# Kernel optimization log

Measured on AMD Instinct MI355X. Metric: run time of the kernel, lower is better.

## Reference

```python
import jax, jax.numpy as jnp
import numpy as np

N = 100000
E = 3200000
IN_C, HID, OUT_C = 256, 32, 16


def gcn_conv(x, W, b, src, dst, n):
    """PyG GCNConv: h = D^{-1/2}(A+I)D^{-1/2} (x W) + b, self-loops already in src/dst."""
    h = x @ W  # [N, out]
    deg = jax.ops.segment_sum(jnp.ones_like(dst, dtype=h.dtype), dst, num_segments=n)
    dinv = jax.lax.rsqrt(deg)  # deg >= 1 because of self-loops
    norm = dinv[src] * dinv[dst]  # [E_all]
    msg = h[src] * norm[:, None]  # gather + normalize
    return jax.ops.segment_sum(msg, dst, num_segments=n) + b


def setup_inputs() -> dict:
    key = jax.random.key(0)
    k1, k2, k3, k4 = jax.random.split(key, 4)
    x = jax.random.normal(k1, (N, IN_C), dtype=jnp.float32)
    edge_index = jax.random.randint(k2, (2, E), 0, N, dtype=jnp.int64)
    # Glorot-ish init for weights, zero bias (as in PyG defaults)
    W1 = jax.random.normal(k3, (IN_C, HID), dtype=jnp.float32) / np.sqrt(IN_C)
    b1 = jnp.zeros((HID,), dtype=jnp.float32)
    W2 = jax.random.normal(k4, (HID, OUT_C), dtype=jnp.float32) / np.sqrt(HID)
    b2 = jnp.zeros((OUT_C,), dtype=jnp.float32)
    return {"x": x, "edge_index": edge_index, "W1": W1, "b1": b1, "W2": W2, "b2": b2}


def reference(x, edge_index, W1, b1, W2, b2):
    n = x.shape[0]
    loops = jnp.arange(n, dtype=edge_index.dtype)
    src = jnp.concatenate([edge_index[0], loops])  # add self-loops
    dst = jnp.concatenate([edge_index[1], loops])
    h = jax.nn.relu(gcn_conv(x, W1, b1, src, dst, n))
    return gcn_conv(h, W2, b2, src, dst, n)
```

## Files before the change

### kernel.cpp

```cpp
#include <hip/hip_runtime.h>

#define IN_C 256
#define HIDC 32
#define OUTC 16
#define NPB  256
#define MAXBKT 800
#define CAP  16384
#define EPB  12288
#define EPT  12

typedef __attribute__((ext_vector_type(8))) short short8;
typedef __attribute__((ext_vector_type(4))) float f32x4;
union S8U4 { short8 s; unsigned u[4]; };

__device__ __forceinline__ unsigned bf16pair(float a, float b) {
    unsigned ua = __float_as_uint(a); ua += 0x7FFF + ((ua >> 16) & 1);
    unsigned ub = __float_as_uint(b); ub += 0x7FFF + ((ub >> 16) & 1);
    return (ua >> 16) | (ub & 0xFFFF0000u);
}
__device__ __forceinline__ float bf16lo(unsigned u) { return __uint_as_float(u << 16); }
__device__ __forceinline__ float bf16hi(unsigned u) { return __uint_as_float(u & 0xFFFF0000u); }
__device__ __forceinline__ unsigned rbf(float a) {
    unsigned u = __float_as_uint(a);
    u += 0x7FFF + ((u >> 16) & 1);
    return u >> 16;
}
__device__ __forceinline__ void split8(const float* xf, short8& hi, short8& lo) {
    S8U4 H, L;
#pragma unroll
    for (int i = 0; i < 4; ++i) {
        float a = xf[2 * i], b = xf[2 * i + 1];
        unsigned ha = rbf(a), hb = rbf(b);
        float ra = a - __uint_as_float(ha << 16);
        float rb = b - __uint_as_float(hb << 16);
        H.u[i] = ha | (hb << 16);
        L.u[i] = rbf(ra) | (rbf(rb) << 16);
    }
    hi = H.s; lo = L.s;
}

__device__ __forceinline__ int edge_at(const int* __restrict__ ei, long long idx, int is64) {
    return is64 ? ei[idx << 1] : ei[idx];
}

__global__ void k_detect(const int* __restrict__ ei, int* __restrict__ flag,
                         int* __restrict__ bkt_cur, int nbkt) {
    __shared__ int nz;
    if (threadIdx.x == 0) nz = 0;
    __syncthreads();
    if (ei[2 * threadIdx.x + 1] != 0) atomicOr(&nz, 1);
    for (int i = threadIdx.x; i < nbkt; i += 256) bkt_cur[i] = i * CAP;
    __syncthreads();
    if (threadIdx.x == 0) *flag = (nz == 0) ? 1 : 0;
}

__global__ __launch_bounds__(1024) void k_bin_scatter(const int* __restrict__ ei, long long E,
                                                      const int* __restrict__ flag,
                                                      int* __restrict__ bkt_cur,
                                                      unsigned* __restrict__ packed, int nbkt) {
    __shared__ int hist[MAXBKT];
    int is64 = *flag;
    for (int i = threadIdx.x; i < nbkt; i += 1024) hist[i] = 0;
    __syncthreads();
    long long lo = (long long)blockIdx.x * EPB;
    int m = (int)((E - lo) < EPB ? (E - lo) : EPB);
    unsigned ew[EPT];
    int      eb[EPT];
#pragma unroll
    for (int j = 0; j < EPT; ++j) {
        int i = j * 1024 + (int)threadIdx.x;
        eb[j] = -1;
        if (i < m) {
            int s = edge_at(ei, lo + i, is64);
            int d = edge_at(ei, E + lo + i, is64);
            ew[j] = (unsigned)s | ((unsigned)(d & (NPB - 1)) << 20);
            eb[j] = d >> 8;
            atomicAdd(&hist[eb[j]], 1);
        }
    }
    __syncthreads();
    for (int b = threadIdx.x; b < nbkt; b += 1024) {
        int c = hist[b];
        hist[b] = c ? atomicAdd(&bkt_cur[b], c) : 0;
    }
    __syncthreads();
#pragma unroll
    for (int j = 0; j < EPT; ++j) {
        if (eb[j] >= 0) {
            int slot = atomicAdd(&hist[eb[j]], 1);
            packed[slot] = ew[j];
        }
    }
}

__global__ __launch_bounds__(256) void k_bucket_csr(const unsigned* __restrict__ packed,
                                                    const int* __restrict__ bkt_cur,
                                                    int* __restrict__ csr_src,
                                                    int* __restrict__ ptr,
                                                    int* __restrict__ cnt,
                                                    float* __restrict__ dinv, int n) {
    __shared__ int hist[NPB];
    __shared__ int off[NPB];
    hist[threadIdx.x] = 0;
    __syncthreads();
    int base = blockIdx.x * CAP;
    int m = bkt_cur[blockIdx.x] - base;
    for (int i = threadIdx.x; i < m; i += 256)
        atomicAdd(&hist[packed[base + i] >> 20], 1);
    __syncthreads();
    off[threadIdx.x] = hist[threadIdx.x];
    __syncthreads();
    for (int o = 1; o < NPB; o <<= 1) {
        int v = (threadIdx.x >= o) ? off[threadIdx.x - o] : 0;
        __syncthreads();
        off[threadIdx.x] += v;
        __syncthreads();
    }
    int node = blockIdx.x * NPB + threadIdx.x;
    {
        int exc = off[threadIdx.x] - hist[threadIdx.x];
        if (node < n) {
            ptr[node]  = base + exc;
            cnt[node]  = hist[threadIdx.x];
            dinv[node] = rsqrtf((float)hist[threadIdx.x] + 1.0f);
        }
        hist[threadIdx.x] = exc;
    }
    __syncthreads();
    for (int i = threadIdx.x; i < m; i += 256) {
        unsigned w = packed[base + i];
        int r = atomicAdd(&hist[w >> 20], 1);
        csr_src[base + r] = (int)(w & 0xFFFFF);
    }
}

__global__ void k_wfrag(const float* __restrict__ W1, unsigned short* __restrict__ wf) {
    int idx = blockIdx.x * 256 + threadIdx.x;
    if (idx >= 8 * 2 * 2 * 64) return;
    int lane = idx & 63;
    int part = (idx >> 6) & 1;
    int tile = (idx >> 7) & 1;
    int s    = idx >> 8;
    int col = tile * 16 + (lane & 15);
    int k0  = s * 32 + (lane >> 4) * 8;
#pragma unroll
    for (int j = 0; j < 8; ++j) {
        float v = W1[(long long)(k0 + j) * HIDC + col];
        unsigned h = rbf(v);
        float r = v - __uint_as_float(h << 16);
        wf[(long long)idx * 8 + j] = (unsigned short)(part == 0 ? h : rbf(r));
    }
}

__global__ __launch_bounds__(256) void k_gemm1(const float* __restrict__ x,
                                               const unsigned short* __restrict__ wf,
                                               const float* __restrict__ dinv,
                                               unsigned short* __restrict__ h1b_us, int n) {
    const int t = threadIdx.x;
    const int l = t & 63;
    const int w = t >> 6;
    const long long nb0 = (long long)blockIdx.x * 64 + w * 16;
    const int arow = l & 15;
    const int kg = l >> 4;
    const long long nodeA = nb0 + arow;
    const bool loadA = nodeA < n;
    f32x4 acc0 = {0.f, 0.f, 0.f, 0.f}, acc1 = {0.f, 0.f, 0.f, 0.f};

#pragma unroll
    for (int s = 0; s < 8; ++s) {
        float xf[8];
        if (loadA) {
            float4 v0 = *(const float4*)(x + nodeA * IN_C + s * 32 + kg * 8);
            float4 v1 = *(const float4*)(x + nodeA * IN_C + s * 32 + kg * 8 + 4);
            xf[0] = v0.x; xf[1] = v0.y; xf[2] = v0.z; xf[3] = v0.w;
            xf[4] = v1.x; xf[5] = v1.y; xf[6] = v1.z; xf[7] = v1.w;
        } else {
#pragma unroll
            for (int j = 0; j < 8; ++j) xf[j] = 0.f;
        }
        short8 ah, al;
        split8(xf, ah, al);
        const unsigned short* base = wf + ((long long)(s * 4) * 64 + l) * 8;
        short8 bh0 = *(const short8*)(base);
        short8 bl0 = *(const short8*)(base + 64 * 8);
        short8 bh1 = *(const short8*)(base + 2 * 64 * 8);
        short8 bl1 = *(const short8*)(base + 3 * 64 * 8);
        acc0 = __builtin_amdgcn_mfma_f32_16x16x32_bf16(ah, bh0, acc0, 0, 0, 0);
        acc0 = __builtin_amdgcn_mfma_f32_16x16x32_bf16(ah, bl0, acc0, 0, 0, 0);
        acc0 = __builtin_amdgcn_mfma_f32_16x16x32_bf16(al, bh0, acc0, 0, 0, 0);
        acc1 = __builtin_amdgcn_mfma_f32_16x16x32_bf16(ah, bh1, acc1, 0, 0, 0);
        acc1 = __builtin_amdgcn_mfma_f32_16x16x32_bf16(ah, bl1, acc1, 0, 0, 0);
        acc1 = __builtin_amdgcn_mfma_f32_16x16x32_bf16(al, bh1, acc1, 0, 0, 0);
    }
#pragma unroll
    for (int r = 0; r < 4; ++r) {
        long long nd = nb0 + (l >> 4) * 4 + r;
        if (nd < n) {
            float di = dinv[nd];
            h1b_us[nd * 32 + (l & 15)]      = (unsigned short)rbf(acc0[r] * di);
            h1b_us[nd * 32 + 16 + (l & 15)] = (unsigned short)rbf(acc1[r] * di);
        }
    }
}

__global__ __launch_bounds__(256) void k_agg1g2(const int* __restrict__ ptr,
                                                const int* __restrict__ cnt,
                                                const int* __restrict__ csr_src,
                                                const float* __restrict__ dinv,
                                                const unsigned* __restrict__ h1b,
                                                const float* __restrict__ b1,
                                                const float* __restrict__ W2,
                                                unsigned* __restrict__ h2b, int n) {
    __shared__ float hs[16][33];
    __shared__ float wl2[32][17];
    const int t = threadIdx.x;
    for (int i = t; i < HIDC * OUTC; i += 256) wl2[i >> 4][i & 15] = W2[i];
    const int nl = t >> 4;
    const int cp = t & 15;
    const long long node = (long long)blockIdx.x * 16 + nl;
    float vL = 0.f, vH = 0.f;
    if (node < n) {
        unsigned us = h1b[node * 16 + cp];
        float accL = bf16lo(us), accH = bf16hi(us);
        int st = ptr[node], deg = cnt[node];
        int j = 0;
        for (; j + 3 < deg; j += 4) {
            int s0 = csr_src[st + j], s1 = csr_src[st + j + 1];
            int s2 = csr_src[st + j + 2], s3 = csr_src[st + j + 3];
            unsigned u0 = h1b[(long long)s0 * 16 + cp];
            unsigned u1 = h1b[(long long)s1 * 16 + cp];
            unsigned u2 = h1b[(long long)s2 * 16 + cp];
            unsigned u3 = h1b[(long long)s3 * 16 + cp];
            accL += (bf16lo(u0) + bf16lo(u1)) + (bf16lo(u2) + bf16lo(u3));
            accH += (bf16hi(u0) + bf16hi(u1)) + (bf16hi(u2) + bf16hi(u3));
        }
        for (; j < deg; ++j) {
            unsigned u = h1b[(long long)csr_src[st + j] * 16 + cp];
            accL += bf16lo(u); accH += bf16hi(u);
        }
        float di = dinv[node];
        vL = accL * di + b1[2 * cp];
        vH = accH * di + b1[2 * cp + 1];
        vL = vL > 0.f ? vL : 0.f;
        vH = vH > 0.f ? vH : 0.f;
    }
    hs[nl][2 * cp]     = vL;
    hs[nl][2 * cp + 1] = vH;
    __syncthreads();
    if (t < 128) {
        int nl2 = t >> 3;
        int op  = t & 7;
        long long nd = (long long)blockIdx.x * 16 + nl2;
        if (nd < n) {
            float o0 = 0.f, o1 = 0.f;
#pragma unroll
            for (int k = 0; k < HIDC; ++k) {
                float h = hs[nl2][k];
                o0 = fmaf(h, wl2[k][2 * op],     o0);
                o1 = fmaf(h, wl2[k][2 * op + 1], o1);
            }
            float di = dinv[nd];
            h2b[nd * 8 + op] = bf16pair(o0 * di, o1 * di);
        }
    }
}

__global__ __launch_bounds__(256) void k_agg2csr(const int* __restrict__ ptr,
                                                 const int* __restrict__ cnt,
                                                 const int* __restrict__ csr_src,
                                                 const float* __restrict__ dinv,
                                                 const unsigned* __restrict__ h2b,
                                                 const float* __restrict__ b2,
                                                 float* __restrict__ out, int n) {
    long long g = (long long)blockIdx.x * blockDim.x + threadIdx.x;
    int node = (int)(g >> 3);
    int cp = (int)(g & 7);
    if (node >= n) return;
    unsigned us = h2b[(long long)node * 8 + cp];
    float accL = bf16lo(us), accH = bf16hi(us);
    int st = ptr[node], deg = cnt[node];
    int j = 0;
    for (; j + 3 < deg; j += 4) {
        int s0 = csr_src[st + j], s1 = csr_src[st + j + 1];
        int s2 = csr_src[st + j + 2], s3 = csr_src[st + j + 3];
        unsigned u0 = h2b[(long long)s0 * 8 + cp];
        unsigned u1 = h2b[(long long)s1 * 8 + cp];
        unsigned u2 = h2b[(long long)s2 * 8 + cp];
        unsigned u3 = h2b[(long long)s3 * 8 + cp];
        accL += (bf16lo(u0) + bf16lo(u1)) + (bf16lo(u2) + bf16lo(u3));
        accH += (bf16hi(u0) + bf16hi(u1)) + (bf16hi(u2) + bf16hi(u3));
    }
    for (; j < deg; ++j) {
        unsigned u = h2b[(long long)csr_src[st + j] * 8 + cp];
        accL += bf16lo(u); accH += bf16hi(u);
    }
    float di = dinv[node];
    *(float2*)(out + (long long)node * OUTC + 2 * cp) =
        make_float2(accL * di + b2[2 * cp], accH * di + b2[2 * cp + 1]);
}

extern "C" void kernel_launch(void* const* d_in, const int* in_sizes, int n_in,
                              void* d_out, int out_size, void* d_ws, size_t ws_size,
                              hipStream_t stream) {
    const float* x  = (const float*)d_in[0];
    const int*   ei = (const int*)d_in[1];
    const float* W1 = (const float*)d_in[2];
    const float* b1 = (const float*)d_in[3];
    const float* W2 = (const float*)d_in[4];
    const float* b2 = (const float*)d_in[5];
    const int n = in_sizes[0] / IN_C;
    const long long E = in_sizes[1] / 2;
    float* out = (float*)d_out;

    const int nbkt = (n + NPB - 1) / NPB;

    char* ws = (char*)d_ws;
    size_t off = 0;
    auto alloc = [&](size_t bytes) { void* p = ws + off; off += (bytes + 255) & ~(size_t)255; return p; };
    int*      flag     = (int*)alloc(256);
    int*      bkt_cur  = (int*)alloc((size_t)MAXBKT * 4);
    float*    dinv     = (float*)alloc((size_t)n * 4);
    int*      cnt      = (int*)alloc((size_t)n * 4);
    int*      ptr      = (int*)alloc((size_t)n * 4);
    unsigned* packed   = (unsigned*)alloc((size_t)nbkt * CAP * 4);
    int*      csr_src  = (int*)alloc((size_t)nbkt * CAP * 4);
    unsigned short* wf = (unsigned short*)alloc(8 * 2 * 2 * 64 * 8 * 2);
    unsigned* h1b      = (unsigned*)alloc((size_t)n * (HIDC / 2) * 4);
    unsigned* h2b      = (unsigned*)alloc((size_t)n * (OUTC / 2) * 4);

    k_detect<<<1, 256, 0, stream>>>(ei, flag, bkt_cur, nbkt);
    k_wfrag<<<8, 256, 0, stream>>>(W1, wf);
    k_bin_scatter<<<(int)((E + EPB - 1) / EPB), 1024, 0, stream>>>(ei, E, flag, bkt_cur, packed, nbkt);
    k_bucket_csr<<<nbkt, NPB, 0, stream>>>(packed, bkt_cur, csr_src, ptr, cnt, dinv, n);

    k_gemm1<<<(n + 63) / 64, 256, 0, stream>>>(x, wf, dinv, (unsigned short*)h1b, n);
    k_agg1g2<<<(n + 15) / 16, 256, 0, stream>>>(ptr, cnt, csr_src, dinv, h1b, b1, W2, h2b, n);
    k_agg2csr<<<(int)(((long long)n * 8 + 255) / 256), 256, 0, stream>>>(
        ptr, cnt, csr_src, dinv, h2b, b2, out, n);
}
```

Measured before the change: 171.7 us.

## Merge edge binning and GEMM1 into one launch; apply dinv scaling in CSR build

Merges k_detect and k_wfrag into a single init kernel. Runs the edge bin-scatter blocks and the x·W1 MFMA GEMM blocks in one combined 1024-thread launch, so the bandwidth-heavy edge scatter and the x streaming can overlap instead of running back to back. Because the GEMM no longer waits for dinv, it writes unscaled bf16 h1. The bucket CSR kernel then rescales each node row by dinv in place, which costs an extra read-modify-write pass over h1 and a second bf16 rounding.

```diff
diff --git a/kernel.cpp b/kernel.cpp
--- a/kernel.cpp
+++ b/kernel.cpp
@@ -43,52 +43,119 @@
     return is64 ? ei[idx << 1] : ei[idx];
 }
 
-__global__ void k_detect(const int* __restrict__ ei, int* __restrict__ flag,
-                         int* __restrict__ bkt_cur, int nbkt) {
-    __shared__ int nz;
-    if (threadIdx.x == 0) nz = 0;
-    __syncthreads();
-    if (ei[2 * threadIdx.x + 1] != 0) atomicOr(&nz, 1);
-    for (int i = threadIdx.x; i < nbkt; i += 256) bkt_cur[i] = i * CAP;
-    __syncthreads();
-    if (threadIdx.x == 0) *flag = (nz == 0) ? 1 : 0;
-}
-
-__global__ __launch_bounds__(1024) void k_bin_scatter(const int* __restrict__ ei, long long E,
-                                                      const int* __restrict__ flag,
-                                                      int* __restrict__ bkt_cur,
-                                                      unsigned* __restrict__ packed, int nbkt) {
-    __shared__ int hist[MAXBKT];
-    int is64 = *flag;
-    for (int i = threadIdx.x; i < nbkt; i += 1024) hist[i] = 0;
-    __syncthreads();
-    long long lo = (long long)blockIdx.x * EPB;
-    int m = (int)((E - lo) < EPB ? (E - lo) : EPB);
-    unsigned ew[EPT];
-    int      eb[EPT];
-#pragma unroll
-    for (int j = 0; j < EPT; ++j) {
-        int i = j * 1024 + (int)threadIdx.x;
-        eb[j] = -1;
-        if (i < m) {
-            int s = edge_at(ei, lo + i, is64);
-            int d = edge_at(ei, E + lo + i, is64);
-            ew[j] = (unsigned)s | ((unsigned)(d & (NPB - 1)) << 20);
-            eb[j] = d >> 8;
-            atomicAdd(&hist[eb[j]], 1);
-        }
-    }
-    __syncthreads();
-    for (int b = threadIdx.x; b < nbkt; b += 1024) {
-        int c = hist[b];
-        hist[b] = c ? atomicAdd(&bkt_cur[b], c) : 0;
-    }
-    __syncthreads();
-#pragma unroll
-    for (int j = 0; j < EPT; ++j) {
-        if (eb[j] >= 0) {
-            int slot = atomicAdd(&hist[eb[j]], 1);
-            packed[slot] = ew[j];
+__global__ void k_init(const int* __restrict__ ei, int* __restrict__ flag,
+                       int* __restrict__ bkt_cur, int nbkt,
+                       const float* __restrict__ W1, unsigned short* __restrict__ wf) {
+    if (blockIdx.x == 0) {
+        __shared__ int nz;
+        if (threadIdx.x == 0) nz = 0;
+        __syncthreads();
+        if (ei[2 * threadIdx.x + 1] != 0) atomicOr(&nz, 1);
+        for (int i = threadIdx.x; i < nbkt; i += 256) bkt_cur[i] = i * CAP;
+        __syncthreads();
+        if (threadIdx.x == 0) *flag = (nz == 0) ? 1 : 0;
+    } else {
+        int idx = (blockIdx.x - 1) * 256 + threadIdx.x;
+        int lane = idx & 63;
+        int part = (idx >> 6) & 1;
+        int tile = (idx >> 7) & 1;
+        int s    = idx >> 8;
+        int col = tile * 16 + (lane & 15);
+        int k0  = s * 32 + (lane >> 4) * 8;
+#pragma unroll
+        for (int j = 0; j < 8; ++j) {
+            float v = W1[(long long)(k0 + j) * HIDC + col];
+            unsigned h = rbf(v);
+            float r = v - __uint_as_float(h << 16);
+            wf[(long long)idx * 8 + j] = (unsigned short)(part == 0 ? h : rbf(r));
+        }
+    }
+}
+
+__global__ __launch_bounds__(1024) void k_super(const int* __restrict__ ei, long long E,
+                                                const int* __restrict__ flag,
+                                                int* __restrict__ bkt_cur,
+                                                unsigned* __restrict__ packed, int nbkt, int nsb,
+                                                const float* __restrict__ x,
+                                                const unsigned short* __restrict__ wf,
+                                                unsigned short* __restrict__ h1b_us, int n) {
+    if ((int)blockIdx.x < nsb) {
+        __shared__ int hist[MAXBKT];
+        int is64 = *flag;
+        for (int i = threadIdx.x; i < nbkt; i += 1024) hist[i] = 0;
+        __syncthreads();
+        long long lo = (long long)blockIdx.x * EPB;
+        int m = (int)((E - lo) < EPB ? (E - lo) : EPB);
+        unsigned ew[EPT];
+        int      eb[EPT];
+#pragma unroll
+        for (int j = 0; j < EPT; ++j) {
+            int i = j * 1024 + (int)threadIdx.x;
+            eb[j] = -1;
+            if (i < m) {
+                int s = edge_at(ei, lo + i, is64);
+                int d = edge_at(ei, E + lo + i, is64);
+                ew[j] = (unsigned)s | ((unsigned)(d & (NPB - 1)) << 20);
+                eb[j] = d >> 8;
+                atomicAdd(&hist[eb[j]], 1);
+            }
+        }
+        __syncthreads();
+        for (int b = threadIdx.x; b < nbkt; b += 1024) {
+            int c = hist[b];
+            hist[b] = c ? atomicAdd(&bkt_cur[b], c) : 0;
+        }
+        __syncthreads();
+#pragma unroll
+        for (int j = 0; j < EPT; ++j) {
+            if (eb[j] >= 0) {
+                int slot = atomicAdd(&hist[eb[j]], 1);
+                packed[slot] = ew[j];
+            }
+        }
+    } else {
+        const int gb = (int)blockIdx.x - nsb;
+        const int t = (int)threadIdx.x;
+        const int l = t & 63;
+        const int w = t >> 6;
+        const long long nb0 = (long long)gb * 256 + w * 16;
+        const int kg = l >> 4;
+        const long long nodeA = nb0 + (l & 15);
+        const bool loadA = nodeA < n;
+        f32x4 acc0 = {0.f, 0.f, 0.f, 0.f}, acc1 = {0.f, 0.f, 0.f, 0.f};
+#pragma unroll
+        for (int s = 0; s < 8; ++s) {
+            float xf[8];
+            if (loadA) {
+                float4 v0 = *(const float4*)(x + nodeA * IN_C + s * 32 + kg * 8);
+                float4 v1 = *(const float4*)(x + nodeA * IN_C + s * 32 + kg * 8 + 4);
+                xf[0] = v0.x; xf[1] = v0.y; xf[2] = v0.z; xf[3] = v0.w;
+                xf[4] = v1.x; xf[5] = v1.y; xf[6] = v1.z; xf[7] = v1.w;
+            } else {
+#pragma unroll
+                for (int j = 0; j < 8; ++j) xf[j] = 0.f;
+            }
+            short8 ah, al;
+            split8(xf, ah, al);
+            const unsigned short* base = wf + ((long long)(s * 4) * 64 + l) * 8;
+            short8 bh0 = *(const short8*)(base);
+            short8 bl0 = *(const short8*)(base + 64 * 8);
+            short8 bh1 = *(const short8*)(base + 2 * 64 * 8);
+            short8 bl1 = *(const short8*)(base + 3 * 64 * 8);
+            acc0 = __builtin_amdgcn_mfma_f32_16x16x32_bf16(ah, bh0, acc0, 0, 0, 0);
+            acc0 = __builtin_amdgcn_mfma_f32_16x16x32_bf16(ah, bl0, acc0, 0, 0, 0);
+            acc0 = __builtin_amdgcn_mfma_f32_16x16x32_bf16(al, bh0, acc0, 0, 0, 0);
+            acc1 = __builtin_amdgcn_mfma_f32_16x16x32_bf16(ah, bh1, acc1, 0, 0, 0);
+            acc1 = __builtin_amdgcn_mfma_f32_16x16x32_bf16(ah, bl1, acc1, 0, 0, 0);
+            acc1 = __builtin_amdgcn_mfma_f32_16x16x32_bf16(al, bh1, acc1, 0, 0, 0);
+        }
+#pragma unroll
+        for (int r = 0; r < 4; ++r) {
+            long long nd = nb0 + (l >> 4) * 4 + r;
+            if (nd < n) {
+                h1b_us[nd * 32 + (l & 15)]      = (unsigned short)rbf(acc0[r]);
+                h1b_us[nd * 32 + 16 + (l & 15)] = (unsigned short)rbf(acc1[r]);
+            }
         }
     }
 }
@@ -98,7 +165,8 @@
                                                     int* __restrict__ csr_src,
                                                     int* __restrict__ ptr,
                                                     int* __restrict__ cnt,
-                                                    float* __restrict__ dinv, int n) {
+                                                    float* __restrict__ dinv,
+                                                    unsigned* __restrict__ h1b, int n) {
     __shared__ int hist[NPB];
     __shared__ int off[NPB];
     hist[threadIdx.x] = 0;
@@ -116,13 +184,20 @@
         off[threadIdx.x] += v;
         __syncthreads();
     }
-    int node = blockIdx.x * NPB + threadIdx.x;
+    long long node = (long long)blockIdx.x * NPB + threadIdx.x;
     {
         int exc = off[threadIdx.x] - hist[threadIdx.x];
         if (node < n) {
+            float di = rsqrtf((float)hist[threadIdx.x] + 1.0f);
             ptr[node]  = base + exc;
             cnt[node]  = hist[threadIdx.x];
-            dinv[node] = rsqrtf((float)hist[threadIdx.x] + 1.0f);
+            dinv[node] = di;
+            unsigned* row = h1b + node * 16;
+#pragma unroll
+            for (int q = 0; q < 16; ++q) {
+                unsigned u = row[q];
+                row[q] = bf16pair(bf16lo(u) * di, bf16hi(u) * di);
+            }
         }
         hist[threadIdx.x] = exc;
     }
@@ -131,75 +206,6 @@
         unsigned w = packed[base + i];
         int r = atomicAdd(&hist[w >> 20], 1);
         csr_src[base + r] = (int)(w & 0xFFFFF);
-    }
-}
-
-__global__ void k_wfrag(const float* __restrict__ W1, unsigned short* __restrict__ wf) {
-    int idx = blockIdx.x * 256 + threadIdx.x;
-    if (idx >= 8 * 2 * 2 * 64) return;
-    int lane = idx & 63;
-    int part = (idx >> 6) & 1;
-    int tile = (idx >> 7) & 1;
-    int s    = idx >> 8;
-    int col = tile * 16 + (lane & 15);
-    int k0  = s * 32 + (lane >> 4) * 8;
-#pragma unroll
-    for (int j = 0; j < 8; ++j) {
-        float v = W1[(long long)(k0 + j) * HIDC + col];
-        unsigned h = rbf(v);
-        float r = v - __uint_as_float(h << 16);
-        wf[(long long)idx * 8 + j] = (unsigned short)(part == 0 ? h : rbf(r));
-    }
-}
-
-__global__ __launch_bounds__(256) void k_gemm1(const float* __restrict__ x,
-                                               const unsigned short* __restrict__ wf,
-                                               const float* __restrict__ dinv,
-                                               unsigned short* __restrict__ h1b_us, int n) {
-    const int t = threadIdx.x;
-    const int l = t & 63;
-    const int w = t >> 6;
-    const long long nb0 = (long long)blockIdx.x * 64 + w * 16;
-    const int arow = l & 15;
-    const int kg = l >> 4;
-    const long long nodeA = nb0 + arow;
-    const bool loadA = nodeA < n;
-    f32x4 acc0 = {0.f, 0.f, 0.f, 0.f}, acc1 = {0.f, 0.f, 0.f, 0.f};
-
-#pragma unroll
-    for (int s = 0; s < 8; ++s) {
-        float xf[8];
-        if (loadA) {
-            float4 v0 = *(const float4*)(x + nodeA * IN_C + s * 32 + kg * 8);
-            float4 v1 = *(const float4*)(x + nodeA * IN_C + s * 32 + kg * 8 + 4);
-            xf[0] = v0.x; xf[1] = v0.y; xf[2] = v0.z; xf[3] = v0.w;
-            xf[4] = v1.x; xf[5] = v1.y; xf[6] = v1.z; xf[7] = v1.w;
-        } else {
-#pragma unroll
-            for (int j = 0; j < 8; ++j) xf[j] = 0.f;
-        }
-        short8 ah, al;
-        split8(xf, ah, al);
-        const unsigned short* base = wf + ((long long)(s * 4) * 64 + l) * 8;
-        short8 bh0 = *(const short8*)(base);
-        short8 bl0 = *(const short8*)(base + 64 * 8);
-        short8 bh1 = *(const short8*)(base + 2 * 64 * 8);
-        short8 bl1 = *(const short8*)(base + 3 * 64 * 8);
-        acc0 = __builtin_amdgcn_mfma_f32_16x16x32_bf16(ah, bh0, acc0, 0, 0, 0);
-        acc0 = __builtin_amdgcn_mfma_f32_16x16x32_bf16(ah, bl0, acc0, 0, 0, 0);
-        acc0 = __builtin_amdgcn_mfma_f32_16x16x32_bf16(al, bh0, acc0, 0, 0, 0);
-        acc1 = __builtin_amdgcn_mfma_f32_16x16x32_bf16(ah, bh1, acc1, 0, 0, 0);
-        acc1 = __builtin_amdgcn_mfma_f32_16x16x32_bf16(ah, bl1, acc1, 0, 0, 0);
-        acc1 = __builtin_amdgcn_mfma_f32_16x16x32_bf16(al, bh1, acc1, 0, 0, 0);
-    }
-#pragma unroll
-    for (int r = 0; r < 4; ++r) {
-        long long nd = nb0 + (l >> 4) * 4 + r;
-        if (nd < n) {
-            float di = dinv[nd];
-            h1b_us[nd * 32 + (l & 15)]      = (unsigned short)rbf(acc0[r] * di);
-            h1b_us[nd * 32 + 16 + (l & 15)] = (unsigned short)rbf(acc1[r] * di);
-        }
     }
 }
 
@@ -313,6 +319,8 @@
     float* out = (float*)d_out;
 
     const int nbkt = (n + NPB - 1) / NPB;
+    const int nsb  = (int)((E + EPB - 1) / EPB);
+    const int ngb  = (n + 255) / 256;
 
     char* ws = (char*)d_ws;
     size_t off = 0;
@@ -328,12 +336,10 @@
     unsigned* h1b      = (unsigned*)alloc((size_t)n * (HIDC / 2) * 4);
     unsigned* h2b      = (unsigned*)alloc((size_t)n * (OUTC / 2) * 4);
 
-    k_detect<<<1, 256, 0, stream>>>(ei, flag, bkt_cur, nbkt);
-    k_wfrag<<<8, 256, 0, stream>>>(W1, wf);
-    k_bin_scatter<<<(int)((E + EPB - 1) / EPB), 1024, 0, stream>>>(ei, E, flag, bkt_cur, packed, nbkt);
-    k_bucket_csr<<<nbkt, NPB, 0, stream>>>(packed, bkt_cur, csr_src, ptr, cnt, dinv, n);
-
-    k_gemm1<<<(n + 63) / 64, 256, 0, stream>>>(x, wf, dinv, (unsigned short*)h1b, n);
+    k_init<<<9, 256, 0, stream>>>(ei, flag, bkt_cur, nbkt, W1, wf);
+    k_super<<<nsb + ngb, 1024, 0, stream>>>(ei, E, flag, bkt_cur, packed, nbkt, nsb,
+                                            x, wf, (unsigned short*)h1b, n);
+    k_bucket_csr<<<nbkt, NPB, 0, stream>>>(packed, bkt_cur, csr_src, ptr, cnt, dinv, h1b, n);
     k_agg1g2<<<(n + 15) / 16, 256, 0, stream>>>(ptr, cnt, csr_src, dinv, h1b, b1, W2, h2b, n);
     k_agg2csr<<<(int)(((long long)n * 8 + 255) / 256), 256, 0, stream>>>(
         ptr, cnt, csr_src, dinv, h2b, b2, out, n);
```

Measured after the change: 161.8 us. 5.7% less time.
